# Kernel optimization log

Hardware: AMD Instinct MI355X
Metric: run time of the kernel (lower is better)

## Reference

```python
import jax, jax.numpy as jnp
import numpy as np

NH, N = 48, 384
CARD, SUB, REPR, ENC = 16, 64, 1024, 1024
POOL_FEAT = 256 * 49


def _head_params(keys, app_size):
    k1, k2, k3 = keys
    W1 = jax.random.normal(k1, (CARD, app_size, SUB), jnp.float32) / np.sqrt(app_size)
    b1 = jnp.zeros((CARD, SUB), jnp.float32)
    W2 = jax.random.normal(k2, (CARD, REPR, SUB), jnp.float32) / np.sqrt(REPR)
    b2 = jnp.zeros((CARD, SUB), jnp.float32)
    W3 = jax.random.normal(k3, (CARD, SUB, REPR), jnp.float32) / np.sqrt(SUB)
    b3 = jnp.zeros((CARD, REPR), jnp.float32)
    return W1, b1, W2, b2, W3, b3


def setup_inputs() -> dict:
    key = jax.random.key(0)
    ks = list(jax.random.split(key, 24))
    d = {}
    d['box_features'] = jax.random.normal(ks[0], (N, POOL_FEAT), jnp.float32)
    d['feat3'] = jax.random.normal(ks[1], (1, 256, 25, 25), jnp.float32)
    d['spatial36'] = jax.random.uniform(ks[2], (NH * N, 36), jnp.float32)
    d['Wbh1'] = jax.random.normal(ks[3], (POOL_FEAT, ENC), jnp.float32) / np.sqrt(POOL_FEAT)
    d['bbh1'] = jnp.zeros(ENC, jnp.float32)
    d['Wbh2'] = jax.random.normal(ks[4], (ENC, ENC), jnp.float32) / np.sqrt(ENC)
    d['bbh2'] = jnp.zeros(ENC, jnp.float32)
    d['Wsp1'] = jax.random.normal(ks[5], (36, 128), jnp.float32) / 6.0
    d['bsp1'] = jnp.zeros(128, jnp.float32)
    d['Wsp2'] = jax.random.normal(ks[6], (128, 256), jnp.float32) / np.sqrt(128)
    d['bsp2'] = jnp.zeros(256, jnp.float32)
    d['Wsp3'] = jax.random.normal(ks[7], (256, REPR), jnp.float32) / 16.0
    d['bsp3'] = jnp.zeros(REPR, jnp.float32)
    d['Wadj'] = jax.random.normal(ks[8], (REPR, 1), jnp.float32) / 32.0
    d['badj'] = jnp.zeros(1, jnp.float32)
    for pre, app, k0 in (('A', 2 * ENC, 9), ('O', ENC, 12), ('S', ENC, 15), ('G', 256, 18)):
        W1, b1, W2, b2, W3, b3 = _head_params(ks[k0:k0 + 3], app)
        d[pre + '1W'], d[pre + '1b'] = W1, b1
        d[pre + '2W'], d[pre + '2b'] = W2, b2
        d[pre + '3W'], d[pre + '3b'] = W3, b3
    d['gln_h'] = jnp.ones(ENC, jnp.float32)
    d['bln_h'] = jnp.zeros(ENC, jnp.float32)
    d['gln_o'] = jnp.ones(ENC, jnp.float32)
    d['bln_o'] = jnp.zeros(ENC, jnp.float32)
    d['n_h'] = NH
    return d


def _attn_head(app, sp, W1, b1, W2, b2, W3, b3):
    # app [P_or_1, A], sp [P, REPR] -> relu(sum_c fc3_c(relu(fc1_c(app)*fc2_c(sp))))
    u = jnp.einsum('pa,cas->cps', app, W1) + b1[:, None, :]
    v = jnp.einsum('ps,csd->cpd', sp, W2) + b2[:, None, :]
    t = jax.nn.relu(u * v)  # broadcasts when app has leading 1
    return jax.nn.relu(jnp.einsum('cpd,cdr->pr', t, W3) + b3.sum(0))


def _msg_obj(app, sp, W1, b1, W2, b2, W3, b3):
    # app [n, ENC], sp [h, n, REPR] -> [h, n, REPR]  (object->subject messages)
    u = jnp.einsum('ne,ces->cns', app, W1) + b1[:, None, :]
    v = jnp.einsum('hns,csd->chnd', sp, W2) + b2[:, None, None, :]
    t = jax.nn.relu(u[:, None, :, :] * v)
    return jnp.einsum('chnd,cdr->hnr', t, W3) + b3.sum(0)


def _msg_hum(app, sp, W1, b1, W2, b2, W3, b3):
    # app [h, ENC], sp [h, n, REPR] -> [n, h, REPR]  (subject->object messages)
    u = jnp.einsum('he,ces->chs', app, W1) + b1[:, None, :]
    v = jnp.einsum('hns,csd->cnhd', sp, W2) + b2[:, None, None, :]
    t = jax.nn.relu(u[:, None, :, :] * v)
    return jnp.einsum('cnhd,cdr->nhr', t, W3) + b3.sum(0)


def _ln(x, g, b):
    mu = x.mean(-1, keepdims=True)
    var = jnp.mean((x - mu) ** 2, -1, keepdims=True)
    return (x - mu) * jax.lax.rsqrt(var + 1e-5) * g + b


def reference(box_features, feat3, spatial36, Wbh1, bbh1, Wbh2, bbh2,
              Wsp1, bsp1, Wsp2, bsp2, Wsp3, bsp3, Wadj, badj,
              A1W, A1b, A2W, A2b, A3W, A3b,
              O1W, O1b, O2W, O2b, O3W, O3b,
              S1W, S1b, S2W, S2b, S3W, S3b,
              G1W, G1b, G2W, G2b, G3W, G3b,
              gln_h, bln_h, gln_o, bln_o, n_h):
    h = int(n_h)
    n = box_features.shape[0]
    gfeat = feat3.mean(axis=(2, 3))  # [1, 256] (AdaptiveAvgPool2d(1) + flatten)
    # box_head MLP
    node = jax.nn.relu(box_features @ Wbh1 + bbh1)
    node = jax.nn.relu(node @ Wbh2 + bbh2)  # [n, ENC]
    # spatial_head MLP
    sp = jax.nn.relu(spatial36 @ Wsp1 + bsp1)
    sp = jax.nn.relu(sp @ Wsp2 + bsp2)
    sp = jax.nn.relu(sp @ Wsp3 + bsp3)  # [h*n, REPR]
    sp_r = sp.reshape(h, n, -1)
    x = np.repeat(np.arange(h), n)  # static pair indices
    y = np.tile(np.arange(n), h)
    h_node = node[:h]
    # one message-passing iteration (num_iter=1)
    pair_app = jnp.concatenate([h_node[x], node[y]], axis=1)  # [h*n, 2*ENC]
    w = _attn_head(pair_app, sp, A1W, A1b, A2W, A2b, A3W, A3b)
    adj = (w @ Wadj + badj).reshape(h, n)
    m_h = jax.nn.relu(jnp.sum(jax.nn.softmax(adj, axis=1)[..., None]
                              * _msg_obj(node, sp_r, O1W, O1b, O2W, O2b, O3W, O3b), axis=1))
    h_node = _ln(h_node + m_h, gln_h, bln_h)
    m_o = jax.nn.relu(jnp.sum(jax.nn.softmax(adj.T, axis=1)[..., None]
                              * _msg_hum(h_node, sp_r, S1W, S1b, S2W, S2b, S3W, S3b), axis=1))
    node = _ln(node + m_o, gln_o, bln_o)
    # static keep mask: drop pairs with identical indices (x != y)
    keep = x != y
    xk, yk = x[keep], y[keep]
    sp_k = sp_r[xk, yk]  # [Pk, REPR]
    f_pair = _attn_head(jnp.concatenate([h_node[xk], node[yk]], axis=1), sp_k,
                        A1W, A1b, A2W, A2b, A3W, A3b)
    f_glob = _attn_head(gfeat, sp_k, G1W, G1b, G2W, G2b, G3W, G3b)
    return jnp.concatenate([f_pair, f_glob], axis=1)  # [Pk, 2*REPR]
```

## Files before the change

### kernel.cpp

```cpp
#include <hip/hip_runtime.h>
#include <math.h>

#define NHH 48
#define NNN 384
#define NP  18432
#define NEC 1024
#define MB1 (1024*1024)

#define BM 128
#define BN 128
#define BK 32
#define KPAD 40

typedef __attribute__((ext_vector_type(8))) short short8v;
typedef __attribute__((ext_vector_type(4))) float f32x4;

__device__ __forceinline__ unsigned short f2bf(float x) {
  unsigned int u = __float_as_uint(x);
  u += 0x7fffu + ((u >> 16) & 1u);
  return (unsigned short)(u >> 16);
}
__device__ __forceinline__ float bf2f(unsigned short b) {
  return __uint_as_float(((unsigned)b) << 16);
}

__global__ __launch_bounds__(256) void convw_k(const float* __restrict__ in,
    unsigned short* __restrict__ out, int inK, int outK, int N, int blocked, int koff)
{
  __shared__ float t[64][65];
  int kb = blockIdx.x * 64, nb = blockIdx.y * 64;
  const float* src; size_t stride;
  if (blocked) { src = in + (size_t)(nb >> 6) * inK * 64; stride = 64; }
  else         { src = in + nb; stride = N; }
  for (int i = threadIdx.x; i < 64 * 64; i += 256) {
    int k = i >> 6, d = i & 63;
    t[d][k] = src[(size_t)(kb + koff + k) * stride + d];
  }
  __syncthreads();
  for (int i = threadIdx.x; i < 64 * 64; i += 256) {
    int d = i >> 6, k = i & 63;
    out[(size_t)(nb + d) * outK + kb + k] = f2bf(t[d][k]);
  }
}

__global__ __launch_bounds__(256) void cvt_k(const float* __restrict__ in,
    unsigned short* __restrict__ out, int n)
{
  int i = (blockIdx.x * 256 + threadIdx.x) * 4;
  if (i < n) {
    float4 v = *(const float4*)(in + i);
    uint2 o;
    o.x = (unsigned)f2bf(v.x) | ((unsigned)f2bf(v.y) << 16);
    o.y = (unsigned)f2bf(v.z) | ((unsigned)f2bf(v.w) << 16);
    *(uint2*)(out + i) = o;
  }
}

__global__ __launch_bounds__(256) void biascat4_k(const float* __restrict__ b0,
    const float* __restrict__ b1, const float* __restrict__ b2,
    const float* __restrict__ b3, float* __restrict__ out)
{
  int j = blockIdx.x * 256 + threadIdx.x;
  if (j < 4096) {
    int g = j >> 10, c = j & 1023;
    const float* b = g == 0 ? b0 : (g == 1 ? b1 : (g == 2 ? b2 : b3));
    out[j] = b[c];
  }
}

template<int MODE, int CBF16>
__global__ __launch_bounds__(256) void gemm_db(
    const unsigned short* __restrict__ A, int lda,
    const unsigned short* __restrict__ B, int ldb,
    void* __restrict__ Cv, int M, int N, int K, int Ks,
    const float* __restrict__ bias, int do_relu,
    const float* __restrict__ x1, const float* __restrict__ x2,
    float* __restrict__ part, int colofs, int swz)
{
  __shared__ unsigned short As[2][BM * KPAD];
  __shared__ unsigned short Bs[2][BN * KPAD];
  __shared__ float red2[BM][2];

  const int tid  = threadIdx.x;
  const int lane = tid & 63;
  const int wave = tid >> 6;
  const int wr = wave >> 1, wc = wave & 1;
  const int lm = lane & 15;
  const int kg = lane >> 4;

  int bx = blockIdx.x, by = blockIdx.y;
  const int bz = blockIdx.z;
  if (swz == 1) {
    int gx = gridDim.x;
    int L = by * gx + bx;
    int r = L & 7, q = L >> 3;
    bx = q % gx;
    by = r + 8 * (q / gx);
  } else if (swz == 3) {
    int gx = gridDim.x;
    int L = by * gx + bx;
    int p = L / 1152, rem = L - p * 1152;
    int r = rem & 7, q = rem >> 3;
    bx = p * 8 + (q & 7);
    by = r + 8 * (q >> 3);
  }

  const unsigned short* Ause = A; int ldause = lda;
  const unsigned short* Buse = B; int ldbuse = ldb;
  const float* biasUse = bias;    int cofs = colofs;
  int bxl = bx;
  if constexpr (MODE == 7) {
    if (bx >= 8) {
      Ause = (const unsigned short*)x1; ldause = 4096;
      Buse = (const unsigned short*)x2; ldbuse = 1024;
      biasUse = part; cofs = 1024;
    }
    bxl = bx & 7;
  }
  const int m0 = by * BM, n0 = bxl * BN;
  const int kbeg = bz * Ks;
  const int kend = min(K, kbeg + Ks);
  const int nt = (kend - kbeg) / BK;

  f32x4 acc[4][4];
#pragma unroll
  for (int i = 0; i < 4; ++i)
#pragma unroll
    for (int j = 0; j < 4; ++j)
      acc[i][j] = (f32x4){0.f, 0.f, 0.f, 0.f};

  const int sr = tid >> 1;
  const int sc = (tid & 1) * 16;
  const unsigned short* aP = Ause + (size_t)(m0 + sr) * ldause + sc;
  const unsigned short* bP = Buse + (size_t)(n0 + sr) * ldbuse + sc;
  const int wofs = sr * KPAD + sc;

  uint4 ra0, ra1, rb0, rb1;
  uint4 sa0, sa1, sb0, sb1;

  auto fetchR = [&](int k0) {
    ra0 = *(const uint4*)(aP + k0); ra1 = *(const uint4*)(aP + k0 + 8);
    rb0 = *(const uint4*)(bP + k0); rb1 = *(const uint4*)(bP + k0 + 8);
  };
  auto fetchS = [&](int k0) {
    sa0 = *(const uint4*)(aP + k0); sa1 = *(const uint4*)(aP + k0 + 8);
    sb0 = *(const uint4*)(bP + k0); sb1 = *(const uint4*)(bP + k0 + 8);
  };
  auto writeR = [&](int buf) {
    *(uint4*)&As[buf][wofs] = ra0; *(uint4*)&As[buf][wofs + 8] = ra1;
    *(uint4*)&Bs[buf][wofs] = rb0; *(uint4*)&Bs[buf][wofs + 8] = rb1;
  };
  auto writeS = [&](int buf) {
    *(uint4*)&As[buf][wofs] = sa0; *(uint4*)&As[buf][wofs + 8] = sa1;
    *(uint4*)&Bs[buf][wofs] = sb0; *(uint4*)&Bs[buf][wofs + 8] = sb1;
  };
  auto computeBuf = [&](const unsigned short* as, const unsigned short* bs) {
    const int lk = kg * 8;
    short8v af[4], bfr[4];
#pragma unroll
    for (int mi = 0; mi < 4; ++mi)
      af[mi] = *(const short8v*)&as[(wr * 64 + mi * 16 + lm) * KPAD + lk];
#pragma unroll
    for (int nj = 0; nj < 4; ++nj)
      bfr[nj] = *(const short8v*)&bs[(wc * 64 + nj * 16 + lm) * KPAD + lk];
#pragma unroll
    for (int mi = 0; mi < 4; ++mi)
#pragma unroll
      for (int nj = 0; nj < 4; ++nj)
        acc[mi][nj] = __builtin_amdgcn_mfma_f32_16x16x32_bf16(af[mi], bfr[nj], acc[mi][nj], 0, 0, 0);
  };

  fetchR(kbeg);
  if (nt > 1) fetchS(kbeg + BK);
  writeR(0);
  if (nt > 2) fetchR(kbeg + 2 * BK);
  __syncthreads();

  for (int it = 0; it < nt; it += 2) {
    writeS(1);
    if (it + 3 < nt) fetchS(kbeg + (it + 3) * BK);
    computeBuf(&As[0][0], &Bs[0][0]);
    __syncthreads();
    if (it + 2 < nt) writeR(0);
    if (it + 4 < nt) fetchR(kbeg + (it + 4) * BK);
    computeBuf(&As[1][0], &Bs[1][0]);
    __syncthreads();
  }

  const int rbase = m0 + wr * 64;
  const int cbase = n0 + wc * 64;

  if constexpr (MODE == 0) {
#pragma unroll
    for (int mi = 0; mi < 4; ++mi)
#pragma unroll
      for (int r = 0; r < 4; ++r) {
        int grow = rbase + mi * 16 + kg * 4 + r;
#pragma unroll
        for (int nj = 0; nj < 4; ++nj) {
          int gcol = cbase + nj * 16 + lm;
          float t = acc[mi][nj][r] + (bias ? bias[gcol] : 0.f);
          float v = do_relu ? fmaxf(t, 0.f) : t;
          size_t idx = (size_t)grow * N + gcol;
          if constexpr (CBF16) ((unsigned short*)Cv)[idx] = f2bf(v);
          else                 ((float*)Cv)[idx] = v;
        }
      }
  } else if constexpr (MODE == 6) {
#pragma unroll
    for (int mi = 0; mi < 4; ++mi)
#pragma unroll
      for (int r = 0; r < 4; ++r) {
        int grow = rbase + mi * 16 + kg * 4 + r;
#pragma unroll
        for (int nj = 0; nj < 4; ++nj) {
          int gcol = cbase + nj * 16 + lm;
          float t = acc[mi][nj][r] + bias[gcol];
          float v = (gcol >= 3072) ? fmaxf(x1[gcol - 3072] * t, 0.f) : t;
          ((unsigned short*)Cv)[(size_t)grow * N + gcol] = f2bf(v);
        }
      }
  } else if constexpr (MODE == 5) {
    size_t zofs = (size_t)bz * M;
#pragma unroll
    for (int mi = 0; mi < 4; ++mi)
#pragma unroll
      for (int r = 0; r < 4; ++r) {
        int grow = rbase + mi * 16 + kg * 4 + r;
#pragma unroll
        for (int nj = 0; nj < 4; ++nj) {
          int gcol = cbase + nj * 16 + lm;
          part[(zofs + grow) * N + gcol] = acc[mi][nj][r];
        }
      }
  } else if constexpr (MODE == 2 || MODE == 7) {
#pragma unroll
    for (int mi = 0; mi < 4; ++mi)
#pragma unroll
      for (int r = 0; r < 4; ++r) {
        int grow = rbase + mi * 16 + kg * 4 + r;
        int h = grow / NNN, n = grow - h * NNN;
        if (n == h) continue;
        long long orow = grow - h - (n > h ? 1 : 0);
#pragma unroll
        for (int nj = 0; nj < 4; ++nj) {
          int gcol = cbase + nj * 16 + lm;
          float v = fmaxf(acc[mi][nj][r] + biasUse[gcol], 0.f);
          ((float*)Cv)[orow * 2048 + cofs + gcol] = v;
        }
      }
  } else if constexpr (MODE == 1) {
#pragma unroll
    for (int mi = 0; mi < 4; ++mi)
#pragma unroll
      for (int r = 0; r < 4; ++r) {
        float s = 0.f;
#pragma unroll
        for (int nj = 0; nj < 4; ++nj) {
          int gcol = cbase + nj * 16 + lm;
          float v = fmaxf(acc[mi][nj][r] + bias[gcol], 0.f);
          s = fmaf(v, x1[gcol], s);
        }
#pragma unroll
        for (int off2 = 1; off2 < 16; off2 <<= 1) s += __shfl_xor(s, off2);
        if (lm == 0) red2[wr * 64 + mi * 16 + kg * 4 + r][wc] = s;
      }
    __syncthreads();
    if (tid < BM) {
      part[(size_t)(m0 + tid) * 8 + bx] = red2[tid][0] + red2[tid][1];
    }
  }
}

__global__ __launch_bounds__(256) void tmulb_k(const unsigned short* __restrict__ vA,
    int vstride, const float* __restrict__ uh, const float* __restrict__ un,
    unsigned short* __restrict__ V)
{
  int p = blockIdx.x;
  int h = p / NNN, n = p - h * NNN;
  int j = threadIdx.x * 4;
  const float* uhr = uh + (size_t)h * NEC + j;
  const float* unr = un + (size_t)n * NEC + j;
  uint2 w = *(const uint2*)(vA + (size_t)p * vstride + j);
  float v0 = bf2f((unsigned short)(w.x & 0xffff));
  float v1 = bf2f((unsigned short)(w.x >> 16));
  float v2 = bf2f((unsigned short)(w.y & 0xffff));
  float v3 = bf2f((unsigned short)(w.y >> 16));
  float f0 = fmaxf((uhr[0] + unr[0]) * v0, 0.f);
  float f1 = fmaxf((uhr[1] + unr[1]) * v1, 0.f);
  float f2 = fmaxf((uhr[2] + unr[2]) * v2, 0.f);
  float f3 = fmaxf((uhr[3] + unr[3]) * v3, 0.f);
  uint2 o;
  o.x = (unsigned)f2bf(f0) | ((unsigned)f2bf(f1) << 16);
  o.y = (unsigned)f2bf(f2) | ((unsigned)f2bf(f3) << 16);
  *(uint2*)(V + (size_t)p * NEC + j) = o;
}

template<int MODE, int ABF16, int BBF16, int CBF16>
__global__ __launch_bounds__(256) void gemm_mfma(
    const void* __restrict__ Av, const void* __restrict__ Bv, long long ldbBlock,
    void* __restrict__ Cv, int M, int N, int K, int Ks,
    const float* __restrict__ bias, int do_relu,
    const float* __restrict__ x1, const float* __restrict__ x2,
    float* __restrict__ part, int colofs, int swz)
{
  __shared__ unsigned short As[BM * KPAD];
  __shared__ unsigned short Bs[BN * KPAD];

  const float* Af = (const float*)Av;
  const unsigned short* Ab = (const unsigned short*)Av;
  const float* Bf = (const float*)Bv;
  const unsigned short* Bb = (const unsigned short*)Bv;

  const int tid  = threadIdx.x;
  const int lane = tid & 63;
  const int wave = tid >> 6;
  const int wr = wave >> 1, wc = wave & 1;
  const int lm = lane & 15;
  const int kg = lane >> 4;

  int bx = blockIdx.x, by = blockIdx.y, bz = blockIdx.z;
  if (swz == 2) {
    int gy = gridDim.y;
    int ntile = gy * gridDim.z;
    int L = (bz * gy + by) * 8 + bx;
    int r = L & 7, q = L >> 3;
    int tpx = ntile >> 3;
    int tile = r * tpx + (q >> 3);
    bx = q & 7;
    bz = tile / gy;
    by = tile - bz * gy;
  }
  const int m0 = by * BM, n0 = bx * BN;
  const int kbeg = bz * Ks;
  const int kend = min(K, kbeg + Ks);

  f32x4 acc[4][4];
#pragma unroll
  for (int i = 0; i < 4; ++i)
#pragma unroll
    for (int j = 0; j < 4; ++j)
      acc[i][j] = (f32x4){0.f, 0.f, 0.f, 0.f};

  const int bn = tid & 127;
  const int kb = (tid >> 7) * 16;
  const float* bsrc = nullptr; long long bstride = 0;
  if constexpr (!BBF16) {
    int gcol = n0 + bn;
    if (ldbBlock) { bsrc = Bf + (long long)(gcol >> 6) * ldbBlock + (gcol & 63); bstride = 64; }
    else          { bsrc = Bf + gcol; bstride = N; }
  }

  uint4 pa0 = {0,0,0,0}, pa1 = {0,0,0,0};
  uint2 qa0 = {0,0}, qa1 = {0,0}, qa2 = {0,0}, qa3 = {0,0};
  uint4 pb0 = {0,0,0,0}, pb1 = {0,0,0,0};

  auto fetchA = [&](int k0) {
    if constexpr (ABF16) {
      int m = tid >> 1, kh = (tid & 1) * 16;
      int gm = m0 + m;
      pa0 = (uint4){0,0,0,0}; pa1 = (uint4){0,0,0,0};
      if (gm < M) {
        const uint4* s = (const uint4*)(Ab + (size_t)gm * K + k0 + kh);
        pa0 = s[0]; pa1 = s[1];
      }
    } else {
#define LOADA_F32(J, DST) { \
      int m = (tid >> 3) + J * 32; int k = (tid & 7) * 4; \
      int gm = m0 + m, gk = k0 + k; \
      float x0=0.f, x1v=0.f, x2v=0.f, x3=0.f; \
      if (gm < M) { const float* src = Af + (long long)gm * K + gk; \
        if (gk + 3 < K) { float4 v = *(const float4*)src; x0=v.x; x1v=v.y; x2v=v.z; x3=v.w; } \
        else { if (gk < K) x0 = src[0]; if (gk+1 < K) x1v = src[1]; \
               if (gk+2 < K) x2v = src[2]; if (gk+3 < K) x3 = src[3]; } } \
      DST.x = (unsigned)f2bf(x0)  | ((unsigned)f2bf(x1v) << 16); \
      DST.y = (unsigned)f2bf(x2v) | ((unsigned)f2bf(x3)  << 16); }
      LOADA_F32(0, qa0) LOADA_F32(1, qa1) LOADA_F32(2, qa2) LOADA_F32(3, qa3)
#undef LOADA_F32
    }
  };
  auto fetchB = [&](int k0) {
    if constexpr (BBF16) {
      int nrow = tid >> 1, kh = (tid & 1) * 16;
      const uint4* s = (const uint4*)(Bb + (size_t)(n0 + nrow) * K + k0 + kh);
      pb0 = s[0]; pb1 = s[1];
    } else {
#define PACKB(I, DST) { int g0 = k0 + kb + 2*I, g1 = g0 + 1; \
      float a = (g0 < K) ? bsrc[(long long)g0 * bstride] : 0.f; \
      float c = (g1 < K) ? bsrc[(long long)g1 * bstride] : 0.f; \
      DST = (unsigned)f2bf(a) | ((unsigned)f2bf(c) << 16); }
      PACKB(0, pb0.x) PACKB(1, pb0.y) PACKB(2, pb0.z) PACKB(3, pb0.w)
      PACKB(4, pb1.x) PACKB(5, pb1.y) PACKB(6, pb1.z) PACKB(7, pb1.w)
#undef PACKB
    }
  };
  auto stage = [&]() {
    if constexpr (ABF16) {
      int m = tid >> 1, kh = (tid & 1) * 16;
      *(uint4*)&As[m * KPAD + kh]     = pa0;
      *(uint4*)&As[m * KPAD + kh + 8] = pa1;
    } else {
      int m = tid >> 3, k = (tid & 7) * 4;
      *(uint2*)&As[(m      ) * KPAD + k] = qa0;
      *(uint2*)&As[(m +  32) * KPAD + k] = qa1;
      *(uint2*)&As[(m +  64) * KPAD + k] = qa2;
      *(uint2*)&As[(m +  96) * KPAD + k] = qa3;
    }
    if constexpr (BBF16) {
      int nrow = tid >> 1, kh = (tid & 1) * 16;
      *(uint4*)&Bs[nrow * KPAD + kh]     = pb0;
      *(uint4*)&Bs[nrow * KPAD + kh + 8] = pb1;
    } else {
      *(uint4*)&Bs[bn * KPAD + kb]     = pb0;
      *(uint4*)&Bs[bn * KPAD + kb + 8] = pb1;
    }
  };

  fetchA(kbeg); fetchB(kbeg);
  for (int k0 = kbeg; k0 < kend; k0 += BK) {
    stage();
    int kn = k0 + BK;
    if (kn < kend) { fetchA(kn); fetchB(kn); }
    __syncthreads();
    {
      const int lk = kg * 8;
      short8v af[4], bfr[4];
#pragma unroll
      for (int mi = 0; mi < 4; ++mi)
        af[mi] = *(const short8v*)&As[(wr * 64 + mi * 16 + lm) * KPAD + lk];
#pragma unroll
      for (int nj = 0; nj < 4; ++nj)
        bfr[nj] = *(const short8v*)&Bs[(wc * 64 + nj * 16 + lm) * KPAD + lk];
#pragma unroll
      for (int mi = 0; mi < 4; ++mi)
#pragma unroll
        for (int nj = 0; nj < 4; ++nj)
          acc[mi][nj] = __builtin_amdgcn_mfma_f32_16x16x32_bf16(af[mi], bfr[nj], acc[mi][nj], 0, 0, 0);
    }
    __syncthreads();
  }

  const int rbase = m0 + wr * 64;
  const int cbase = n0 + wc * 64;

  if constexpr (MODE == 0) {
#pragma unroll
    for (int mi = 0; mi < 4; ++mi)
#pragma unroll
      for (int r = 0; r < 4; ++r) {
        int grow = rbase + mi * 16 + kg * 4 + r;
        if (grow >= M) continue;
#pragma unroll
        for (int nj = 0; nj < 4; ++nj) {
          int gcol = cbase + nj * 16 + lm;
          float t = acc[mi][nj][r] + (bias ? bias[gcol] : 0.f);
          float v = do_relu ? fmaxf(t, 0.f) : t;
          size_t idx = (size_t)grow * N + gcol;
          if constexpr (CBF16) ((unsigned short*)Cv)[idx] = f2bf(v);
          else                 ((float*)Cv)[idx] = v;
        }
      }
  } else if constexpr (MODE == 5) {
    size_t zofs = (size_t)bz * M;
#pragma unroll
    for (int mi = 0; mi < 4; ++mi)
#pragma unroll
      for (int r = 0; r < 4; ++r) {
        int grow = rbase + mi * 16 + kg * 4 + r;
        if (grow >= M) continue;
#pragma unroll
        for (int nj = 0; nj < 4; ++nj) {
          int gcol = cbase + nj * 16 + lm;
          part[(zofs + grow) * N + gcol] = acc[mi][nj][r];
        }
      }
  }
}

__global__ __launch_bounds__(256) void ksum_k(const float* __restrict__ P,
    const float* __restrict__ bias, int do_relu, float* __restrict__ Cf,
    unsigned short* __restrict__ Cb, int MN, int N, int S)
{
  int i = blockIdx.x * 256 + threadIdx.x;
  if (i < MN) {
    float s = 0.f;
    for (int z = 0; z < S; ++z) s += P[(size_t)z * MN + i];
    if (bias) s += bias[i % N];
    float v = do_relu ? fmaxf(s, 0.f) : s;
    if (Cf) Cf[i] = v;
    if (Cb) Cb[i] = f2bf(v);
  }
}

__global__ __launch_bounds__(256) void ksumg_k(const float* __restrict__ P,
    const float* __restrict__ b0, const float* __restrict__ b1, const float* __restrict__ b2,
    float* __restrict__ C0, float* __restrict__ C1, float* __restrict__ C2,
    int M, int NG, int S)
{
  int i = blockIdx.x * 256 + threadIdx.x;
  int N = NG << 10;
  int total = M * N;
  if (i < total) {
    int m = i / N, c = i - m * N;
    int g = c >> 10, col = c & 1023;
    float s = 0.f;
    for (int z = 0; z < S; ++z) s += P[(size_t)z * total + i];
    const float* b = g == 0 ? b0 : (g == 1 ? b1 : b2);
    if (b) s += b[col];
    float* C = g == 0 ? C0 : (g == 1 ? C1 : C2);
    C[(size_t)m * 1024 + col] = s;
  }
}

__global__ __launch_bounds__(256) void tw_k(const unsigned short* __restrict__ V, int sV,
    const float* __restrict__ uO, const float* __restrict__ soft, float* __restrict__ tw)
{
  int h = blockIdx.x;
  int j = blockIdx.y * 256 + threadIdx.x;
  const float* srow = soft + h * NNN;
  float s = 0.f;
  for (int n = 0; n < NNN; ++n) {
    float v = bf2f(V[((size_t)h * NNN + n) * sV + j]);
    float t = fmaxf(uO[(size_t)n * NEC + j] * v, 0.f);
    s = fmaf(srow[n], t, s);
  }
  tw[(size_t)h * NEC + j] = s;
}

__global__ __launch_bounds__(256) void two_k(const unsigned short* __restrict__ V, int sV,
    const float* __restrict__ uS, const float* __restrict__ softT, float* __restrict__ two)
{
  int n = blockIdx.x;
  int j = blockIdx.y * 256 + threadIdx.x;
  const float* srow = softT + n * NHH;
  float s = 0.f;
#pragma unroll 8
  for (int h = 0; h < NHH; ++h) {
    float v = bf2f(V[((size_t)h * NNN + n) * sV + j]);
    float t = fmaxf(uS[(size_t)h * NEC + j] * v, 0.f);
    s = fmaf(srow[h], t, s);
  }
  two[(size_t)n * NEC + j] = s;
}

__global__ void adjfin_k(const float* __restrict__ part, const float* __restrict__ badj,
                         float* __restrict__ adj)
{
  int p = blockIdx.x * blockDim.x + threadIdx.x;
  if (p < NP) {
    float s = badj[0];
#pragma unroll
    for (int c = 0; c < 8; ++c) s += part[(size_t)p * 8 + c];
    adj[p] = s;
  }
}

__global__ __launch_bounds__(64) void softmax_row_k(const float* __restrict__ adj,
                                                    float* __restrict__ soft)
{
  __shared__ float buf[NNN];
  int h = blockIdx.x, t = threadIdx.x;
  float mx = -1e30f;
  for (int n = t; n < NNN; n += 64) { float v = adj[h * NNN + n]; buf[n] = v; mx = fmaxf(mx, v); }
#pragma unroll
  for (int off = 32; off >= 1; off >>= 1) mx = fmaxf(mx, __shfl_xor(mx, off));
  float s = 0.f;
  for (int n = t; n < NNN; n += 64) { float e = expf(buf[n] - mx); buf[n] = e; s += e; }
#pragma unroll
  for (int off = 32; off >= 1; off >>= 1) s += __shfl_xor(s, off);
  float inv = 1.f / s;
  for (int n = t; n < NNN; n += 64) soft[h * NNN + n] = buf[n] * inv;
}

__global__ __launch_bounds__(64) void softmaxT_k(const float* __restrict__ adj,
                                                 float* __restrict__ softT)
{
  int n = blockIdx.x, t = threadIdx.x;
  float v = (t < NHH) ? adj[t * NNN + n] : -1e30f;
  float mx = v;
#pragma unroll
  for (int off = 32; off >= 1; off >>= 1) mx = fmaxf(mx, __shfl_xor(mx, off));
  float e = (t < NHH) ? expf(v - mx) : 0.f;
  float s = e;
#pragma unroll
  for (int off = 32; off >= 1; off >>= 1) s += __shfl_xor(s, off);
  if (t < NHH) softT[n * NHH + t] = e / s;
}

__global__ __launch_bounds__(256) void ln_k(const float* __restrict__ x, const float* __restrict__ m,
    const float* __restrict__ g, const float* __restrict__ b, float* __restrict__ out,
    unsigned short* __restrict__ outb)
{
  int r = blockIdx.x, t = threadIdx.x;
  __shared__ float rs[4], rs2[4];
  const float* xr = x + (size_t)r * NEC;
  const float* mr = m + (size_t)r * NEC;
  float s = 0.f, s2 = 0.f;
  for (int j = t; j < NEC; j += 256) { float v = xr[j] + mr[j]; s += v; s2 = fmaf(v, v, s2); }
#pragma unroll
  for (int off = 32; off >= 1; off >>= 1) { s += __shfl_xor(s, off); s2 += __shfl_xor(s2, off); }
  if ((t & 63) == 0) { rs[t >> 6] = s; rs2[t >> 6] = s2; }
  __syncthreads();
  s = rs[0] + rs[1] + rs[2] + rs[3];
  s2 = rs2[0] + rs2[1] + rs2[2] + rs2[3];
  float mean = s * (1.f / NEC);
  float var = s2 * (1.f / NEC) - mean * mean;
  float rstd = rsqrtf(var + 1e-5f);
  float* o = out + (size_t)r * NEC;
  unsigned short* ob = outb ? outb + (size_t)r * NEC : nullptr;
  for (int j = t; j < NEC; j += 256) {
    float v = xr[j] + mr[j];
    float w = (v - mean) * rstd * g[j] + b[j];
    o[j] = w;
    if (ob) ob[j] = f2bf(w);
  }
}

__global__ __launch_bounds__(64) void gfeat_k(const float* __restrict__ feat3,
                                              float* __restrict__ gfeat)
{
  int ch = blockIdx.x, t = threadIdx.x;
  float s = 0.f;
  for (int i = t; i < 625; i += 64) s += feat3[ch * 625 + i];
#pragma unroll
  for (int off = 32; off >= 1; off >>= 1) s += __shfl_xor(s, off);
  if (t == 0) gfeat[ch] = s * (1.f / 625.f);
}

__global__ __launch_bounds__(256) void b3sum_k(const float* __restrict__ b3,
                                               float* __restrict__ out)
{
  int r = blockIdx.x * 256 + threadIdx.x;
  if (r < NEC) {
    float s = 0.f;
#pragma unroll
    for (int c = 0; c < 16; ++c) s += b3[c * NEC + r];
    out[r] = s;
  }
}

extern "C" void kernel_launch(void* const* d_in, const int* in_sizes, int n_in,
                              void* d_out, int out_size, void* d_ws, size_t ws_size,
                              hipStream_t stream)
{
  const float* box   = (const float*)d_in[0];
  const float* feat3 = (const float*)d_in[1];
  const float* sp36  = (const float*)d_in[2];
  const float* Wbh1  = (const float*)d_in[3];
  const float* bbh1  = (const float*)d_in[4];
  const float* Wbh2  = (const float*)d_in[5];
  const float* bbh2  = (const float*)d_in[6];
  const float* Wsp1  = (const float*)d_in[7];
  const float* bsp1  = (const float*)d_in[8];
  const float* Wsp2  = (const float*)d_in[9];
  const float* bsp2  = (const float*)d_in[10];
  const float* Wsp3  = (const float*)d_in[11];
  const float* bsp3  = (const float*)d_in[12];
  const float* Wadj  = (const float*)d_in[13];
  const float* badj  = (const float*)d_in[14];
  const float* A1W = (const float*)d_in[15]; const float* A1b = (const float*)d_in[16];
  const float* A2W = (const float*)d_in[17]; const float* A2b = (const float*)d_in[18];
  const float* A3W = (const float*)d_in[19]; const float* A3b = (const float*)d_in[20];
  const float* O1W = (const float*)d_in[21]; const float* O1b = (const float*)d_in[22];
  const float* O2W = (const float*)d_in[23]; const float* O2b = (const float*)d_in[24];
  const float* O3W = (const float*)d_in[25]; const float* O3b = (const float*)d_in[26];
  const float* S1W = (const float*)d_in[27]; const float* S1b = (const float*)d_in[28];
  const float* S2W = (const float*)d_in[29]; const float* S2b = (const float*)d_in[30];
  const float* S3W = (const float*)d_in[31]; const float* S3b = (const float*)d_in[32];
  const float* G1W = (const float*)d_in[33]; const float* G1b = (const float*)d_in[34];
  const float* G2W = (const float*)d_in[35]; const float* G2b = (const float*)d_in[36];
  const float* G3W = (const float*)d_in[37]; const float* G3b = (const float*)d_in[38];
  const float* gln_h = (const float*)d_in[39]; const float* bln_h = (const float*)d_in[40];
  const float* gln_o = (const float*)d_in[41]; const float* bln_o = (const float*)d_in[42];
  (void)in_sizes; (void)n_in; (void)out_size; (void)ws_size;

  char* base = (char*)d_ws;
  unsigned short* V4  = (unsigned short*)base;
  float* partialV4    = (float*)base;
  unsigned short* Vb  = (unsigned short*)(base + (size_t)NP * 4096 * 2);
  float* partialVb    = (float*)Vb;
  unsigned short* s1  = Vb;
  unsigned short* s2  = Vb + (size_t)NP * 128;
  unsigned short* SPb = Vb + (size_t)NP * 1024;
  float* f = (float*)(SPb + (size_t)NP * 1024);
  size_t off = 0;
  auto alloc = [&](size_t n) { float* p = f + off; off += n; return p; };
  float* node1 = alloc(384 * NEC);
  float* node  = alloc(384 * NEC);
  float* hnode1= alloc(128 * NEC);
  float* node2 = alloc(384 * NEC);
  float* uhA   = alloc(384 * NEC);
  float* unA   = alloc(384 * NEC);
  float* uO    = alloc(384 * NEC);
  float* uS    = alloc(128 * NEC);
  float* uh2   = alloc(128 * NEC);
  float* un2   = alloc(384 * NEC);
  float* uG    = alloc(NEC);
  float* gfeat = alloc(256);
  float* b3A = alloc(NEC); float* b3O = alloc(NEC); float* b3S = alloc(NEC); float* b3G = alloc(NEC);
  float* bias4 = alloc(4096);
  float* part  = alloc((size_t)NP * 8);
  float* adj   = alloc(NP);
  float* soft  = alloc(NP);
  float* softT = alloc(NP);
  float* twb   = alloc(48 * NEC);
  float* twob  = alloc(384 * NEC);
  float* m_h   = alloc(48 * NEC);
  float* m_o   = alloc(384 * NEC);
  unsigned short* wb = (unsigned short*)(f + off);
  size_t wo = 0;
  auto walloc = [&](size_t n) { unsigned short* p = wb + wo; wo += n; return p; };
  unsigned short* W4b   = walloc((size_t)4 * MB1);
  unsigned short* A3Wb  = walloc((size_t)MB1);
  unsigned short* G3Wb  = walloc((size_t)MB1);
  unsigned short* Wsp3b = walloc((size_t)NEC * 256);
  unsigned short* Wsp2b = walloc((size_t)256 * 128);
  unsigned short* Wbh1b = walloc((size_t)NEC * 12544);
  unsigned short* Wbh2b = walloc((size_t)MB1);
  unsigned short* U1b   = walloc((size_t)3 * MB1);
  unsigned short* U2b   = walloc((size_t)2 * MB1);
  unsigned short* boxb  = walloc((size_t)384 * 12544);
  unsigned short* nodeb = walloc((size_t)384 * NEC);
  unsigned short* node1b= walloc((size_t)384 * NEC);
  unsigned short* hnode1b = walloc((size_t)128 * NEC);
  unsigned short* node2b  = walloc((size_t)384 * NEC);

  auto convw = [&](const float* W, unsigned short* out, int inK, int outK, int N,
                   int blocked, int koff) {
    dim3 g(outK / 64, N / 64);
    hipLaunchKernelGGL(convw_k, g, dim3(256), 0, stream, W, out, inK, outK, N, blocked, koff);
  };
  auto gS = [&](const float* A, const float* B, long long lb, float* C,
                int M, int N, int K, const float* bias, int relu, int S) {
    int Ks = ((K + S * BK - 1) / (S * BK)) * BK;
    dim3 grid(N / BN, (M + BM - 1) / BM, S);
    hipLaunchKernelGGL((gemm_mfma<5, 0, 0, 0>), grid, dim3(256), 0, stream,
                       A, B, lb, nullptr, M, N, K, Ks, nullptr, 0,
                       nullptr, nullptr, partialVb, 0, 2);
    int MN = M * N;
    hipLaunchKernelGGL(ksum_k, dim3((MN + 255) / 256), dim3(256), 0, stream,
                       partialVb, bias, relu, C, (unsigned short*)nullptr, MN, N, S);
  };

  convw(A2W, W4b + 0 * MB1, NEC, NEC, NEC, 1, 0);
  convw(O2W, W4b + 1 * MB1, NEC, NEC, NEC, 1, 0);
  convw(S2W, W4b + 2 * MB1, NEC, NEC, NEC, 1, 0);
  convw(G2W, W4b + 3 * MB1, NEC, NEC, NEC, 1, 0);
  convw(A3W, A3Wb, NEC, NEC, NEC, 0, 0);
  convw(G3W, G3Wb, NEC, NEC, NEC, 0, 0);
  convw(Wsp3, Wsp3b, 256, 256, NEC, 0, 0);
  convw(Wsp2, Wsp2b, 128, 128, 256, 0, 0);
  convw(Wbh1, Wbh1b, 12544, 12544, NEC, 0, 0);
  convw(Wbh2, Wbh2b, NEC, NEC, NEC, 0, 0);
  convw(A1W, U1b + 0 * MB1, 2048, NEC, NEC, 1, 0);
  convw(A1W, U1b + 1 * MB1, 2048, NEC, NEC, 1, 1024);
  convw(O1W, U1b + 2 * MB1, NEC, NEC, NEC, 1, 0);
  convw(S1W, U2b + 0 * MB1, NEC, NEC, NEC, 1, 0);
  convw(A1W, U2b + 1 * MB1, 2048, NEC, NEC, 1, 0);
  cvt_k<<<(384 * 12544 / 4 + 255) / 256, 256, 0, stream>>>(box, boxb, 384 * 12544);

  gfeat_k<<<256, 64, 0, stream>>>(feat3, gfeat);
  b3sum_k<<<4, 256, 0, stream>>>(A3b, b3A);
  b3sum_k<<<4, 256, 0, stream>>>(O3b, b3O);
  b3sum_k<<<4, 256, 0, stream>>>(S3b, b3S);
  b3sum_k<<<4, 256, 0, stream>>>(G3b, b3G);
  biascat4_k<<<16, 256, 0, stream>>>(A2b, O2b, S2b, G2b, bias4);

  {
    dim3 grid(8, 3, 28);
    hipLaunchKernelGGL((gemm_db<5, 0>), grid, dim3(256), 0, stream,
                       boxb, 12544, Wbh1b, 12544, nullptr, 384, NEC, 12544, 448,
                       nullptr, 0, nullptr, nullptr, partialV4, 0, 0);
    hipLaunchKernelGGL(ksum_k, dim3((384 * NEC + 255) / 256), dim3(256), 0, stream,
                       partialV4, bbh1, 1, (float*)nullptr, node1b, 384 * NEC, NEC, 28);
  }
  {
    dim3 grid(8, 3, 8);
    hipLaunchKernelGGL((gemm_db<5, 0>), grid, dim3(256), 0, stream,
                       node1b, NEC, Wbh2b, NEC, nullptr, 384, NEC, NEC, 128,
                       nullptr, 0, nullptr, nullptr, partialV4, 0, 0);
    hipLaunchKernelGGL(ksum_k, dim3((384 * NEC + 255) / 256), dim3(256), 0, stream,
                       partialV4, bbh2, 1, node, nodeb, 384 * NEC, NEC, 8);
  }

  {
    dim3 g1(1, NP / BM);
    hipLaunchKernelGGL((gemm_mfma<0, 0, 0, 1>), g1, dim3(256), 0, stream,
                       sp36, Wsp1, 0LL, s1, NP, 128, 36, 36, bsp1, 1, nullptr, nullptr, nullptr, 0, 0);
    dim3 g2(2, NP / BM);
    hipLaunchKernelGGL((gemm_db<0, 1>), g2, dim3(256), 0, stream,
                       s1, 128, Wsp2b, 128, s2, NP, 256, 128, 128, bsp2, 1,
                       nullptr, nullptr, nullptr, 0, 0);
    dim3 g3(8, NP / BM);
    hipLaunchKernelGGL((gemm_db<0, 1>), g3, dim3(256), 0, stream,
                       s2, 256, Wsp3b, 256, SPb, NP, NEC, 256, 256, bsp3, 1,
                       nullptr, nullptr, nullptr, 0, 1);
  }

  {
    dim3 g1(8, 1);
    hipLaunchKernelGGL((gemm_mfma<0, 0, 0, 0>), g1, dim3(256), 0, stream,
                       gfeat, G1W, 256LL * 64, uG, 1, NEC, 256, 256, G1b, 0,
                       nullptr, nullptr, nullptr, 0, 0);
  }

  {
    dim3 grid(32, NP / BM);
    hipLaunchKernelGGL((gemm_db<6, 1>), grid, dim3(256), 0, stream,
                       SPb, NEC, W4b, NEC, V4, NP, 4096, NEC, NEC,
                       bias4, 0, uG, nullptr, nullptr, 0, 3);
  }

  {
    dim3 grid(24, 3, 8);
    hipLaunchKernelGGL((gemm_db<5, 0>), grid, dim3(256), 0, stream,
                       nodeb, NEC, U1b, NEC, nullptr, 384, 3072, NEC, 128,
                       nullptr, 0, nullptr, nullptr, partialVb, 0, 0);
    int total = 384 * 3072;
    hipLaunchKernelGGL(ksumg_k, dim3((total + 255) / 256), dim3(256), 0, stream,
                       partialVb, A1b, (const float*)nullptr, O1b, uhA, unA, uO, 384, 3, 8);
  }

  tmulb_k<<<NP, 256, 0, stream>>>(V4 + 0, 4096, uhA, unA, Vb);
  {
    dim3 g(8, NP / BM);
    hipLaunchKernelGGL((gemm_db<1, 0>), g, dim3(256), 0, stream,
                       Vb, NEC, A3Wb, NEC, nullptr, NP, NEC, NEC, NEC,
                       b3A, 1, Wadj, nullptr, part, 0, 1);
  }
  adjfin_k<<<(NP + 255) / 256, 256, 0, stream>>>(part, badj, adj);
  softmax_row_k<<<NHH, 64, 0, stream>>>(adj, soft);
  softmaxT_k<<<NNN, 64, 0, stream>>>(adj, softT);

  tw_k<<<dim3(NHH, 4), 256, 0, stream>>>(V4 + 1024, 4096, uO, soft, twb);
  gS(twb, O3W, 0, m_h, 48, NEC, NEC, b3O, 1, 16);
  ln_k<<<NHH, 256, 0, stream>>>(node, m_h, gln_h, bln_h, hnode1, hnode1b);

  {
    dim3 grid(16, 1, 8);
    hipLaunchKernelGGL((gemm_db<5, 0>), grid, dim3(256), 0, stream,
                       hnode1b, NEC, U2b, NEC, nullptr, 128, 2048, NEC, 128,
                       nullptr, 0, nullptr, nullptr, partialVb, 0, 0);
    int total = 128 * 2048;
    hipLaunchKernelGGL(ksumg_k, dim3((total + 255) / 256), dim3(256), 0, stream,
                       partialVb, S1b, A1b, (const float*)nullptr, uS, uh2, (float*)nullptr, 128, 2, 8);
  }

  two_k<<<dim3(NNN, 4), 256, 0, stream>>>(V4 + 2048, 4096, uS, softT, twob);
  gS(twob, S3W, 0, m_o, 384, NEC, NEC, b3S, 1, 16);
  ln_k<<<NNN, 256, 0, stream>>>(node, m_o, gln_o, bln_o, node2, node2b);

  {
    dim3 grid(8, 3, 8);
    hipLaunchKernelGGL((gemm_db<5, 0>), grid, dim3(256), 0, stream,
                       node2b, NEC, U1b + 1 * MB1, NEC, nullptr, 384, NEC, NEC, 128,
                       nullptr, 0, nullptr, nullptr, partialVb, 0, 0);
    hipLaunchKernelGGL(ksum_k, dim3((384 * NEC + 255) / 256), dim3(256), 0, stream,
                       partialVb, (const float*)nullptr, 0, un2, (unsigned short*)nullptr, 384 * NEC, NEC, 8);
  }

  tmulb_k<<<NP, 256, 0, stream>>>(V4 + 0, 4096, uh2, un2, Vb);

  {
    dim3 g(16, NP / BM);
    hipLaunchKernelGGL((gemm_db<7, 0>), g, dim3(256), 0, stream,
                       Vb, NEC, A3Wb, NEC, (float*)d_out, NP, NEC, NEC, NEC,
                       b3A, 1, (const float*)(V4 + 3072), (const float*)G3Wb,
                       b3G, 0, 3);
  }
}
```

Measured before the change: 823.0 us.

## Fuse pair elementwise product into A-operand load of A3 GEMMs; batch weight conversions

Removes the two tmulb_k passes that materialised relu((uh+un)*V) as a bf16 matrix. That transform now happens while the A tile is loaded inside the MODE 1 and MODE 7 GEMMs, which read V4 directly with stride 4096. This avoids writing and rereading an 18432x1024 bf16 buffer twice. It also batches the twelve 1024-wide weight transposes into one launch and the four bias sums into one launch to cut launch overhead. The cost is extra global loads of uh/un rows and extra ALU work in the GEMM load path, which may slow the main loop.

```diff
diff --git a/kernel.cpp b/kernel.cpp
--- a/kernel.cpp
+++ b/kernel.cpp
@@ -43,6 +43,35 @@
   }
 }
 
+struct CJobs {
+  const float* src[12];
+  unsigned short* dst[12];
+  int inK[12];
+  int koff[12];
+  int blocked[12];
+};
+__global__ __launch_bounds__(256) void convjobs_k(CJobs J)
+{
+  __shared__ float t[64][65];
+  int z = blockIdx.z;
+  const float* in = J.src[z];
+  unsigned short* out = J.dst[z];
+  int inK = J.inK[z], koff = J.koff[z], blocked = J.blocked[z];
+  int kb = blockIdx.x * 64, nb = blockIdx.y * 64;
+  const float* src; size_t stride;
+  if (blocked) { src = in + (size_t)(nb >> 6) * inK * 64; stride = 64; }
+  else         { src = in + nb; stride = NEC; }
+  for (int i = threadIdx.x; i < 64 * 64; i += 256) {
+    int k = i >> 6, d = i & 63;
+    t[d][k] = src[(size_t)(kb + koff + k) * stride + d];
+  }
+  __syncthreads();
+  for (int i = threadIdx.x; i < 64 * 64; i += 256) {
+    int d = i >> 6, k = i & 63;
+    out[(size_t)(nb + d) * NEC + kb + k] = f2bf(t[d][k]);
+  }
+}
+
 __global__ __launch_bounds__(256) void cvt_k(const float* __restrict__ in,
     unsigned short* __restrict__ out, int n)
 {
@@ -56,6 +85,20 @@
   }
 }
 
+struct Ptr4 { const float* s[4]; float* d[4]; };
+__global__ __launch_bounds__(256) void b3sum4_k(Ptr4 P)
+{
+  int r = blockIdx.x * 256 + threadIdx.x;
+  const float* b3 = P.s[blockIdx.y];
+  float* out = P.d[blockIdx.y];
+  if (r < NEC) {
+    float s = 0.f;
+#pragma unroll
+    for (int c = 0; c < 16; ++c) s += b3[c * NEC + r];
+    out[r] = s;
+  }
+}
+
 __global__ __launch_bounds__(256) void biascat4_k(const float* __restrict__ b0,
     const float* __restrict__ b1, const float* __restrict__ b2,
     const float* __restrict__ b3, float* __restrict__ out)
@@ -75,6 +118,7 @@
     void* __restrict__ Cv, int M, int N, int K, int Ks,
     const float* __restrict__ bias, int do_relu,
     const float* __restrict__ x1, const float* __restrict__ x2,
+    const float* __restrict__ uh, const float* __restrict__ un,
     float* __restrict__ part, int colofs, int swz)
 {
   __shared__ unsigned short As[2][BM * KPAD];
@@ -109,11 +153,14 @@
   const unsigned short* Buse = B; int ldbuse = ldb;
   const float* biasUse = bias;    int cofs = colofs;
   int bxl = bx;
+  bool afuse = (MODE == 1);
   if constexpr (MODE == 7) {
     if (bx >= 8) {
       Ause = (const unsigned short*)x1; ldause = 4096;
       Buse = (const unsigned short*)x2; ldbuse = 1024;
       biasUse = part; cofs = 1024;
+    } else {
+      afuse = true;
     }
     bxl = bx & 7;
   }
@@ -135,15 +182,55 @@
   const unsigned short* bP = Buse + (size_t)(n0 + sr) * ldbuse + sc;
   const int wofs = sr * KPAD + sc;
 
+  const float* uhr = nullptr; const float* unr = nullptr;
+  if constexpr (MODE == 1 || MODE == 7) {
+    int grow = m0 + sr;
+    int hh = grow / NNN, nn = grow - hh * NNN;
+    uhr = uh + (size_t)hh * NEC;
+    unr = un + (size_t)nn * NEC;
+  }
+
   uint4 ra0, ra1, rb0, rb1;
   uint4 sa0, sa1, sb0, sb1;
 
+  auto loadA = [&](int k0, uint4& o0, uint4& o1) {
+    if constexpr (MODE == 1 || MODE == 7) {
+      if (afuse) {
+        int cc = k0 + sc;
+        uint4 va = *(const uint4*)(aP + k0);
+        uint4 vb2 = *(const uint4*)(aP + k0 + 8);
+        float s[16];
+#pragma unroll
+        for (int q = 0; q < 4; ++q) {
+          float4 a4 = *(const float4*)(uhr + cc + q * 4);
+          float4 b4 = *(const float4*)(unr + cc + q * 4);
+          s[q * 4 + 0] = a4.x + b4.x; s[q * 4 + 1] = a4.y + b4.y;
+          s[q * 4 + 2] = a4.z + b4.z; s[q * 4 + 3] = a4.w + b4.w;
+        }
+        unsigned w[8] = {va.x, va.y, va.z, va.w, vb2.x, vb2.y, vb2.z, vb2.w};
+        unsigned o[8];
+#pragma unroll
+        for (int q = 0; q < 8; ++q) {
+          float e0 = bf2f((unsigned short)(w[q] & 0xffff));
+          float e1 = bf2f((unsigned short)(w[q] >> 16));
+          float r0 = fmaxf(s[2 * q] * e0, 0.f);
+          float r1 = fmaxf(s[2 * q + 1] * e1, 0.f);
+          o[q] = (unsigned)f2bf(r0) | ((unsigned)f2bf(r1) << 16);
+        }
+        o0 = (uint4){o[0], o[1], o[2], o[3]};
+        o1 = (uint4){o[4], o[5], o[6], o[7]};
+        return;
+      }
+    }
+    o0 = *(const uint4*)(aP + k0);
+    o1 = *(const uint4*)(aP + k0 + 8);
+  };
   auto fetchR = [&](int k0) {
-    ra0 = *(const uint4*)(aP + k0); ra1 = *(const uint4*)(aP + k0 + 8);
+    loadA(k0, ra0, ra1);
     rb0 = *(const uint4*)(bP + k0); rb1 = *(const uint4*)(bP + k0 + 8);
   };
   auto fetchS = [&](int k0) {
-    sa0 = *(const uint4*)(aP + k0); sa1 = *(const uint4*)(aP + k0 + 8);
+    loadA(k0, sa0, sa1);
     sb0 = *(const uint4*)(bP + k0); sb1 = *(const uint4*)(bP + k0 + 8);
   };
   auto writeR = [&](int buf) {
@@ -233,7 +320,7 @@
           part[(zofs + grow) * N + gcol] = acc[mi][nj][r];
         }
       }
-  } else if constexpr (MODE == 2 || MODE == 7) {
+  } else if constexpr (MODE == 7) {
 #pragma unroll
     for (int mi = 0; mi < 4; ++mi)
 #pragma unroll
@@ -270,30 +357,6 @@
       part[(size_t)(m0 + tid) * 8 + bx] = red2[tid][0] + red2[tid][1];
     }
   }
-}
-
-__global__ __launch_bounds__(256) void tmulb_k(const unsigned short* __restrict__ vA,
-    int vstride, const float* __restrict__ uh, const float* __restrict__ un,
-    unsigned short* __restrict__ V)
-{
-  int p = blockIdx.x;
-  int h = p / NNN, n = p - h * NNN;
-  int j = threadIdx.x * 4;
-  const float* uhr = uh + (size_t)h * NEC + j;
-  const float* unr = un + (size_t)n * NEC + j;
-  uint2 w = *(const uint2*)(vA + (size_t)p * vstride + j);
-  float v0 = bf2f((unsigned short)(w.x & 0xffff));
-  float v1 = bf2f((unsigned short)(w.x >> 16));
-  float v2 = bf2f((unsigned short)(w.y & 0xffff));
-  float v3 = bf2f((unsigned short)(w.y >> 16));
-  float f0 = fmaxf((uhr[0] + unr[0]) * v0, 0.f);
-  float f1 = fmaxf((uhr[1] + unr[1]) * v1, 0.f);
-  float f2 = fmaxf((uhr[2] + unr[2]) * v2, 0.f);
-  float f3 = fmaxf((uhr[3] + unr[3]) * v3, 0.f);
-  uint2 o;
-  o.x = (unsigned)f2bf(f0) | ((unsigned)f2bf(f1) << 16);
-  o.y = (unsigned)f2bf(f2) | ((unsigned)f2bf(f3) << 16);
-  *(uint2*)(V + (size_t)p * NEC + j) = o;
 }
 
 template<int MODE, int ABF16, int BBF16, int CBF16>
@@ -625,18 +688,6 @@
 #pragma unroll
   for (int off = 32; off >= 1; off >>= 1) s += __shfl_xor(s, off);
   if (t == 0) gfeat[ch] = s * (1.f / 625.f);
-}
-
-__global__ __launch_bounds__(256) void b3sum_k(const float* __restrict__ b3,
-                                               float* __restrict__ out)
-{
-  int r = blockIdx.x * 256 + threadIdx.x;
-  if (r < NEC) {
-    float s = 0.f;
-#pragma unroll
-    for (int c = 0; c < 16; ++c) s += b3[c * NEC + r];
-    out[r] = s;
-  }
 }
 
 extern "C" void kernel_launch(void* const* d_in, const int* in_sizes, int n_in,
@@ -742,35 +793,40 @@
                        partialVb, bias, relu, C, (unsigned short*)nullptr, MN, N, S);
   };
 
-  convw(A2W, W4b + 0 * MB1, NEC, NEC, NEC, 1, 0);
-  convw(O2W, W4b + 1 * MB1, NEC, NEC, NEC, 1, 0);
-  convw(S2W, W4b + 2 * MB1, NEC, NEC, NEC, 1, 0);
-  convw(G2W, W4b + 3 * MB1, NEC, NEC, NEC, 1, 0);
-  convw(A3W, A3Wb, NEC, NEC, NEC, 0, 0);
-  convw(G3W, G3Wb, NEC, NEC, NEC, 0, 0);
+  {
+    CJobs J;
+    J.src[0]=A2W;  J.dst[0]=W4b+0*MB1;   J.inK[0]=1024; J.koff[0]=0;    J.blocked[0]=1;
+    J.src[1]=O2W;  J.dst[1]=W4b+1*MB1;   J.inK[1]=1024; J.koff[1]=0;    J.blocked[1]=1;
+    J.src[2]=S2W;  J.dst[2]=W4b+2*MB1;   J.inK[2]=1024; J.koff[2]=0;    J.blocked[2]=1;
+    J.src[3]=G2W;  J.dst[3]=W4b+3*MB1;   J.inK[3]=1024; J.koff[3]=0;    J.blocked[3]=1;
+    J.src[4]=A1W;  J.dst[4]=U1b+0*MB1;   J.inK[4]=2048; J.koff[4]=0;    J.blocked[4]=1;
+    J.src[5]=A1W;  J.dst[5]=U1b+1*MB1;   J.inK[5]=2048; J.koff[5]=1024; J.blocked[5]=1;
+    J.src[6]=O1W;  J.dst[6]=U1b+2*MB1;   J.inK[6]=1024; J.koff[6]=0;    J.blocked[6]=1;
+    J.src[7]=S1W;  J.dst[7]=U2b+0*MB1;   J.inK[7]=1024; J.koff[7]=0;    J.blocked[7]=1;
+    J.src[8]=A1W;  J.dst[8]=U2b+1*MB1;   J.inK[8]=2048; J.koff[8]=0;    J.blocked[8]=1;
+    J.src[9]=A3W;  J.dst[9]=A3Wb;        J.inK[9]=1024; J.koff[9]=0;    J.blocked[9]=0;
+    J.src[10]=G3W; J.dst[10]=G3Wb;       J.inK[10]=1024;J.koff[10]=0;   J.blocked[10]=0;
+    J.src[11]=Wbh2;J.dst[11]=Wbh2b;      J.inK[11]=1024;J.koff[11]=0;   J.blocked[11]=0;
+    hipLaunchKernelGGL(convjobs_k, dim3(16, 16, 12), dim3(256), 0, stream, J);
+  }
   convw(Wsp3, Wsp3b, 256, 256, NEC, 0, 0);
   convw(Wsp2, Wsp2b, 128, 128, 256, 0, 0);
   convw(Wbh1, Wbh1b, 12544, 12544, NEC, 0, 0);
-  convw(Wbh2, Wbh2b, NEC, NEC, NEC, 0, 0);
-  convw(A1W, U1b + 0 * MB1, 2048, NEC, NEC, 1, 0);
-  convw(A1W, U1b + 1 * MB1, 2048, NEC, NEC, 1, 1024);
-  convw(O1W, U1b + 2 * MB1, NEC, NEC, NEC, 1, 0);
-  convw(S1W, U2b + 0 * MB1, NEC, NEC, NEC, 1, 0);
-  convw(A1W, U2b + 1 * MB1, 2048, NEC, NEC, 1, 0);
   cvt_k<<<(384 * 12544 / 4 + 255) / 256, 256, 0, stream>>>(box, boxb, 384 * 12544);
 
   gfeat_k<<<256, 64, 0, stream>>>(feat3, gfeat);
-  b3sum_k<<<4, 256, 0, stream>>>(A3b, b3A);
-  b3sum_k<<<4, 256, 0, stream>>>(O3b, b3O);
-  b3sum_k<<<4, 256, 0, stream>>>(S3b, b3S);
-  b3sum_k<<<4, 256, 0, stream>>>(G3b, b3G);
+  {
+    Ptr4 P; P.s[0]=A3b; P.s[1]=O3b; P.s[2]=S3b; P.s[3]=G3b;
+    P.d[0]=b3A; P.d[1]=b3O; P.d[2]=b3S; P.d[3]=b3G;
+    hipLaunchKernelGGL(b3sum4_k, dim3(4, 4), dim3(256), 0, stream, P);
+  }
   biascat4_k<<<16, 256, 0, stream>>>(A2b, O2b, S2b, G2b, bias4);
 
   {
     dim3 grid(8, 3, 28);
     hipLaunchKernelGGL((gemm_db<5, 0>), grid, dim3(256), 0, stream,
                        boxb, 12544, Wbh1b, 12544, nullptr, 384, NEC, 12544, 448,
-                       nullptr, 0, nullptr, nullptr, partialV4, 0, 0);
+                       nullptr, 0, nullptr, nullptr, nullptr, nullptr, partialV4, 0, 0);
     hipLaunchKernelGGL(ksum_k, dim3((384 * NEC + 255) / 256), dim3(256), 0, stream,
                        partialV4, bbh1, 1, (float*)nullptr, node1b, 384 * NEC, NEC, 28);
   }
@@ -778,7 +834,7 @@
     dim3 grid(8, 3, 8);
     hipLaunchKernelGGL((gemm_db<5, 0>), grid, dim3(256), 0, stream,
                        node1b, NEC, Wbh2b, NEC, nullptr, 384, NEC, NEC, 128,
-                       nullptr, 0, nullptr, nullptr, partialV4, 0, 0);
+                       nullptr, 0, nullptr, nullptr, nullptr, nullptr, partialV4, 0, 0);
     hipLaunchKernelGGL(ksum_k, dim3((384 * NEC + 255) / 256), dim3(256), 0, stream,
                        partialV4, bbh2, 1, node, nodeb, 384 * NEC, NEC, 8);
   }
@@ -790,11 +846,11 @@
     dim3 g2(2, NP / BM);
     hipLaunchKernelGGL((gemm_db<0, 1>), g2, dim3(256), 0, stream,
                        s1, 128, Wsp2b, 128, s2, NP, 256, 128, 128, bsp2, 1,
-                       nullptr, nullptr, nullptr, 0, 0);
+                       nullptr, nullptr, nullptr, nullptr, nullptr, 0, 0);
     dim3 g3(8, NP / BM);
     hipLaunchKernelGGL((gemm_db<0, 1>), g3, dim3(256), 0, stream,
                        s2, 256, Wsp3b, 256, SPb, NP, NEC, 256, 256, bsp3, 1,
-                       nullptr, nullptr, nullptr, 0, 1);
+                       nullptr, nullptr, nullptr, nullptr, nullptr, 0, 1);
   }
 
   {
@@ -808,25 +864,24 @@
     dim3 grid(32, NP / BM);
     hipLaunchKernelGGL((gemm_db<6, 1>), grid, dim3(256), 0, stream,
                        SPb, NEC, W4b, NEC, V4, NP, 4096, NEC, NEC,
-                       bias4, 0, uG, nullptr, nullptr, 0, 3);
+                       bias4, 0, uG, nullptr, nullptr, nullptr, nullptr, 0, 3);
   }
 
   {
     dim3 grid(24, 3, 8);
     hipLaunchKernelGGL((gemm_db<5, 0>), grid, dim3(256), 0, stream,
                        nodeb, NEC, U1b, NEC, nullptr, 384, 3072, NEC, 128,
-                       nullptr, 0, nullptr, nullptr, partialVb, 0, 0);
+                       nullptr, 0, nullptr, nullptr, nullptr, nullptr, partialVb, 0, 0);
     int total = 384 * 3072;
     hipLaunchKernelGGL(ksumg_k, dim3((total + 255) / 256), dim3(256), 0, stream,
                        partialVb, A1b, (const float*)nullptr, O1b, uhA, unA, uO, 384, 3, 8);
   }
 
-  tmulb_k<<<NP, 256, 0, stream>>>(V4 + 0, 4096, uhA, unA, Vb);
   {
     dim3 g(8, NP / BM);
     hipLaunchKernelGGL((gemm_db<1, 0>), g, dim3(256), 0, stream,
-                       Vb, NEC, A3Wb, NEC, nullptr, NP, NEC, NEC, NEC,
-                       b3A, 1, Wadj, nullptr, part, 0, 1);
+                       V4 + 0, 4096, A3Wb, NEC, nullptr, NP, NEC, NEC, NEC,
+                       b3A, 1, Wadj, nullptr, uhA, unA, part, 0, 1);
   }
   adjfin_k<<<(NP + 255) / 256, 256, 0, stream>>>(part, badj, adj);
   softmax_row_k<<<NHH, 64, 0, stream>>>(adj, soft);
@@ -840,7 +895,7 @@
     dim3 grid(16, 1, 8);
     hipLaunchKernelGGL((gemm_db<5, 0>), grid, dim3(256), 0, stream,
                        hnode1b, NEC, U2b, NEC, nullptr, 128, 2048, NEC, 128,
-                       nullptr, 0, nullptr, nullptr, partialVb, 0, 0);
+                       nullptr, 0, nullptr, nullptr, nullptr, nullptr, partialVb, 0, 0);
     int total = 128 * 2048;
     hipLaunchKernelGGL(ksumg_k, dim3((total + 255) / 256), dim3(256), 0, stream,
                        partialVb, S1b, A1b, (const float*)nullptr, uS, uh2, (float*)nullptr, 128, 2, 8);
@@ -854,18 +909,16 @@
     dim3 grid(8, 3, 8);
     hipLaunchKernelGGL((gemm_db<5, 0>), grid, dim3(256), 0, stream,
                        node2b, NEC, U1b + 1 * MB1, NEC, nullptr, 384, NEC, NEC, 128,
-                       nullptr, 0, nullptr, nullptr, partialVb, 0, 0);
+                       nullptr, 0, nullptr, nullptr, nullptr, nullptr, partialVb, 0, 0);
     hipLaunchKernelGGL(ksum_k, dim3((384 * NEC + 255) / 256), dim3(256), 0, stream,
                        partialVb, (const float*)nullptr, 0, un2, (unsigned short*)nullptr, 384 * NEC, NEC, 8);
   }
 
-  tmulb_k<<<NP, 256, 0, stream>>>(V4 + 0, 4096, uh2, un2, Vb);
-
   {
     dim3 g(16, NP / BM);
     hipLaunchKernelGGL((gemm_db<7, 0>), g, dim3(256), 0, stream,
-                       Vb, NEC, A3Wb, NEC, (float*)d_out, NP, NEC, NEC, NEC,
+                       V4 + 0, 4096, A3Wb, NEC, (float*)d_out, NP, NEC, NEC, NEC,
                        b3A, 1, (const float*)(V4 + 3072), (const float*)G3Wb,
-                       b3G, 0, 3);
-  }
-}
+                       uh2, un2, b3G, 0, 3);
+  }
+}
```

After: 866.0 us. +5.2%, slower.
